# Performance work log

Hardware: AMD Instinct MI355X
Metric: run time of the kernel (lower is better)

Reference implementation:

```python
import jax, jax.numpy as jnp
import numpy as np

B = 8192
D1 = 1024
D2 = 1024
H = 4096  # subnet hidden width
SCALE_LIMIT = 1.0


def _mlp(x, W1, b1, W2, b2):
    # Linear -> ReLU -> Linear
    return jnp.maximum(x @ W1 + b1, 0.0) @ W2 + b2


def setup_inputs() -> dict:
    key = jax.random.key(0)
    ks = jax.random.split(key, 17)
    inp = {"x": jax.random.normal(ks[0], (B, D1 + D2), dtype=jnp.float32)}
    # four subnets: s1,t1 map d2->d1 ; s2,t2 map d1->d2
    specs = {"s1": (D2, D1), "t1": (D2, D1), "s2": (D1, D2), "t2": (D1, D2)}
    i = 1
    for name, (din, dout) in specs.items():
        inp[f"{name}_W1"] = 0.02 * jax.random.normal(ks[i], (din, H), dtype=jnp.float32); i += 1
        inp[f"{name}_b1"] = jnp.zeros((H,), dtype=jnp.float32)
        inp[f"{name}_W2"] = 0.02 * jax.random.normal(ks[i], (H, dout), dtype=jnp.float32); i += 1
        inp[f"{name}_b2"] = jnp.zeros((dout,), dtype=jnp.float32)
    return inp


def reference(x,
              s1_W1, s1_b1, s1_W2, s1_b2,
              t1_W1, t1_b1, t1_W2, t1_b2,
              s2_W1, s2_b1, s2_W2, s2_b2,
              t2_W1, t2_b1, t2_W2, t2_b2):
    x1, x2 = x[:, :D1], x[:, D1:]
    # first half-step: update x1 conditioned on x2
    s2v = jnp.tanh(_mlp(x2, s1_W1, s1_b1, s1_W2, s1_b2)) * SCALE_LIMIT  # [B, D1]
    t2v = _mlp(x2, t1_W1, t1_b1, t1_W2, t1_b2)                          # [B, D1]
    y1 = x1 * jnp.exp(s2v) + t2v
    # second half-step: update x2 conditioned on y1
    s1v = jnp.tanh(_mlp(y1, s2_W1, s2_b1, s2_W2, s2_b2)) * SCALE_LIMIT  # [B, D2]
    t1v = _mlp(y1, t2_W1, t2_b1, t2_W2, t2_b2)                          # [B, D2]
    y2 = x2 * jnp.exp(s1v) + t1v
    y = jnp.concatenate([y1, y2], axis=1)  # [B, D1+D2]
    # exact triangular-coupling log-det (what the autograd loop computes per-sample)
    log_det = jnp.sum(s2v, axis=1) + jnp.sum(s1v, axis=1)  # [B]
    return y, log_det
```

## Files before the change

### kernel.cpp

```cpp
#include <hip/hip_runtime.h>
#include <cstdint>
#include <cstddef>

#define BDIM 8192
#define D1 1024
#define HDIM 4096

typedef __attribute__((ext_vector_type(8))) short short8;
typedef __attribute__((ext_vector_type(4))) float f32x4;
typedef __attribute__((ext_vector_type(4))) unsigned short u16x4;

__device__ inline void async_load16(const void* g, void* l) {
  __builtin_amdgcn_global_load_lds(
      (const __attribute__((address_space(1))) void*)g,
      (__attribute__((address_space(3))) void*)l,
      16 , 0 , 0 );
}

__device__ inline unsigned short f2bf(float f) {
  union { float f; uint32_t u; } v; v.f = f;
  uint32_t u = v.u;
  uint32_t r = u + 0x7FFFu + ((u >> 16) & 1u);
  return (unsigned short)(r >> 16);
}
__device__ inline float bf2f(unsigned short u) {
  union { uint32_t u; float f; } v; v.u = (uint32_t)u << 16; return v.f;
}

__global__ __launch_bounds__(512, 2)
void gemm8(const unsigned short* __restrict__ A0,
           const unsigned short* __restrict__ A1, int lda,
           const unsigned short* __restrict__ B0,
           const unsigned short* __restrict__ B1,
           const float* __restrict__ bias0, const float* __restrict__ bias1,
           unsigned short* __restrict__ C0, unsigned short* __restrict__ C1,
           int ldc, int K, int relu) {
  __shared__ __align__(16) unsigned short smem[65536];

  const int z = blockIdx.z;
  const unsigned short* A  = z ? A1 : A0;
  const unsigned short* Bw = z ? B1 : B0;
  const float* biasP       = z ? bias1 : bias0;
  unsigned short* C        = z ? C1 : C0;

  const int nX  = gridDim.x;
  const int nwg = gridDim.x * gridDim.y;
  const int bid = blockIdx.y * gridDim.x + blockIdx.x;
  const int q = nwg >> 3, r = nwg & 7;
  const int xcd = bid & 7, rest = bid >> 3;
  const int wg = (xcd < r ? xcd * (q + 1) : r * (q + 1) + (xcd - r) * q) + rest;
  const int tm = wg / nX, tn = wg % nX;
  const int m0 = tm * 256, n0 = tn * 256;

  const int tid  = threadIdx.x;
  const int wave = tid >> 6, lane = tid & 63;
  const int quad = lane >> 4, l15 = lane & 15;
  const int wm = wave >> 2, wn = wave & 3;

  const int sr    = tid >> 2;
  const int sslot = (tid & 3) ^ ((tid >> 3) & 3);
  const unsigned short* gA = A  + (long)(m0 + sr) * lda + sslot * 8;
  const unsigned short* gB = Bw + (long)(n0 + sr) * K   + sslot * 8;

  const int rdoff = l15 * 32 + ((quad ^ ((l15 >> 1) & 3)) << 3);

  f32x4 acc[8][4] = {};
  const int NT = K >> 5;

#define STAGE_A(SB, KT) { \
  unsigned short* lw = smem + (SB)*8192 + wave*512; \
  const unsigned short* g = gA + (long)(KT)*32; \
  async_load16(g, lw); \
  async_load16(g + 128*(long)lda, lw + 4096); }

#define STAGE_B(SB, KT) { \
  unsigned short* lw = smem + 32768 + (SB)*8192 + wave*512; \
  const unsigned short* g = gB + (long)(KT)*32; \
  async_load16(g, lw); \
  async_load16(g + 128*(long)K, lw + 4096); }

#define READ_AL(d, BUF) { \
  const unsigned short* p = smem + (BUF)*8192 + wm*4096 + rdoff; \
  d[0] = *(const short8*)(p);        d[1] = *(const short8*)(p + 512); \
  d[2] = *(const short8*)(p + 1024); d[3] = *(const short8*)(p + 1536); }

#define READ_AH(d, BUF) { \
  const unsigned short* p = smem + (BUF)*8192 + wm*4096 + 2048 + rdoff; \
  d[0] = *(const short8*)(p);        d[1] = *(const short8*)(p + 512); \
  d[2] = *(const short8*)(p + 1024); d[3] = *(const short8*)(p + 1536); }

#define READ_B(d, BUF) { \
  const unsigned short* p = smem + 32768 + (BUF)*8192 + wn*2048 + rdoff; \
  d[0] = *(const short8*)(p);        d[1] = *(const short8*)(p + 512); \
  d[2] = *(const short8*)(p + 1024); d[3] = *(const short8*)(p + 1536); }

#define MFMA16L(AV, BV) \
  _Pragma("unroll") \
  for (int mt = 0; mt < 4; ++mt) { \
    _Pragma("unroll") \
    for (int nt = 0; nt < 4; ++nt) { \
      acc[mt][nt] = __builtin_amdgcn_mfma_f32_16x16x32_bf16( \
          AV[mt], BV[nt], acc[mt][nt], 0, 0, 0); \
    } }

#define MFMA16H(AV, BV) \
  _Pragma("unroll") \
  for (int mt = 0; mt < 4; ++mt) { \
    _Pragma("unroll") \
    for (int nt = 0; nt < 4; ++nt) { \
      acc[4 + mt][nt] = __builtin_amdgcn_mfma_f32_16x16x32_bf16( \
          AV[mt], BV[nt], acc[4 + mt][nt], 0, 0, 0); \
    } }

#define BARRIER() asm volatile("s_barrier" ::: "memory")
#define VMCNT8()  asm volatile("s_waitcnt vmcnt(8)" ::: "memory")

#define STEP(BUF, SB, KTS, CA, CB, NA, NBv) { \
  short8 h4[4]; \
  READ_AH(h4, BUF); \
  { const int kt = (KTS) < NT ? (KTS) : NT - 1; \
    STAGE_A(SB, kt); STAGE_B(SB, kt); } \
  __builtin_amdgcn_s_setprio(1); MFMA16L(CA, CB); __builtin_amdgcn_s_setprio(0); \
  VMCNT8(); \
  BARRIER(); \
  READ_AL(NA, ((BUF) + 1) & 3); READ_B(NBv, ((BUF) + 1) & 3); \
  __builtin_amdgcn_s_setprio(1); MFMA16H(h4, CB); __builtin_amdgcn_s_setprio(0); \
}

  short8 pa[4], pb[4], qa[4], qb[4];

  STAGE_A(0, 0); STAGE_B(0, 0);
  STAGE_A(1, 1); STAGE_B(1, 1);
  STAGE_A(2, 2); STAGE_B(2, 2);
  VMCNT8();
  BARRIER();
  READ_AL(pa, 0); READ_B(pb, 0);

#pragma unroll 1
  for (int t = 0; t < NT; t += 4) {
    STEP(0, 3, t + 3, pa, pb, qa, qb);
    STEP(1, 0, t + 4, qa, qb, pa, pb);
    STEP(2, 1, t + 5, pa, pb, qa, qb);
    STEP(3, 2, t + 6, qa, qb, pa, pb);
  }

  asm volatile("s_waitcnt vmcnt(0)" ::: "memory");
  BARRIER();

  unsigned short* sc = smem + wave * 8192;
#pragma unroll
  for (int nt = 0; nt < 4; ++nt) {
    const int col = n0 + wn * 64 + nt * 16 + l15;
    const float bv = biasP[col];
#pragma unroll
    for (int mt = 0; mt < 8; ++mt) {
#pragma unroll
      for (int rr = 0; rr < 4; ++rr) {
        const int lrow = mt * 16 + quad * 4 + rr;
        float v = acc[mt][nt][rr] + bv;
        if (relu) v = v > 0.f ? v : 0.f;
        sc[lrow * 64 + ((nt * 16 + l15) ^ (((lrow >> 2) & 3) << 4))] = f2bf(v);
      }
    }
  }
  const long rowbase = m0 + wm * 128;
  const int colbase  = n0 + wn * 64;
#pragma unroll
  for (int i = 0; i < 16; ++i) {
    const int L   = i * 1024 + lane * 16;
    const int row = L >> 7;
    const int sp  = (L & 127) >> 4;
    const int cg  = sp ^ ((((row) >> 2) & 3) << 1);
    short8 v = *(const short8*)&sc[row * 64 + sp * 8];
    *(short8*)&C[(rowbase + row) * (long)ldc + colbase + cg * 8] = v;
  }

#undef STAGE_A
#undef STAGE_B
#undef READ_AL
#undef READ_AH
#undef READ_B
#undef MFMA16L
#undef MFMA16H
#undef BARRIER
#undef VMCNT8
#undef STEP
}

__global__ __launch_bounds__(256)
void couple(const unsigned short* sb, const unsigned short* __restrict__ tb,
            const float* __restrict__ x, float* __restrict__ y,
            unsigned short* y1b, float* __restrict__ ld,
            long growoff, int xoff, int addld) {
  __shared__ float wsum[4];
  const int row = blockIdx.x;
  const long grow = growoff + row;
  const int c = threadIdx.x * 4;

  u16x4 sv4 = *(const u16x4*)&sb[(long)row * 1024 + c];
  u16x4 tv4 = *(const u16x4*)&tb[(long)row * 1024 + c];
  f32x4 xv  = *(const f32x4*)&x[grow * 2048 + xoff + c];
  f32x4 yv;
  unsigned short yb[4];
  float rs = 0.f;
#pragma unroll
  for (int j = 0; j < 4; ++j) {
    float s  = bf2f(sv4[j]);
    float t  = bf2f(tv4[j]);
    float sv = tanhf(s);
    rs += sv;
    float yy = xv[j] * __expf(sv) + t;
    yv[j] = yy;
    yb[j] = f2bf(yy);
  }
  *(f32x4*)&y[grow * 2048 + xoff + c] = yv;
  if (y1b) {
    u16x4 o; o[0] = yb[0]; o[1] = yb[1]; o[2] = yb[2]; o[3] = yb[3];
    *(u16x4*)&y1b[(long)row * 1024 + c] = o;
  }
#pragma unroll
  for (int o = 32; o > 0; o >>= 1) rs += __shfl_down(rs, o);
  const int wv = threadIdx.x >> 6, ln = threadIdx.x & 63;
  if (ln == 0) wsum[wv] = rs;
  __syncthreads();
  if (threadIdx.x == 0) {
    float tot = wsum[0] + wsum[1] + wsum[2] + wsum[3];
    if (addld) ld[grow] += tot; else ld[grow] = tot;
  }
}

__global__ __launch_bounds__(256)
void transpose_cast4(const float* __restrict__ s0, const float* __restrict__ s1,
                     const float* __restrict__ s2, const float* __restrict__ s3,
                     unsigned short* __restrict__ d0, unsigned short* __restrict__ d1,
                     unsigned short* __restrict__ d2, unsigned short* __restrict__ d3,
                     int R, int C) {
  __shared__ float tile[32][33];
  const int bz = blockIdx.z;
  const float* in = bz == 0 ? s0 : bz == 1 ? s1 : bz == 2 ? s2 : s3;
  unsigned short* out = bz == 0 ? d0 : bz == 1 ? d1 : bz == 2 ? d2 : d3;
  const int bx = blockIdx.x * 32;
  const int by = blockIdx.y * 32;
  const int tx = threadIdx.x & 31;
  const int ty = threadIdx.x >> 5;
  for (int j = ty; j < 32; j += 8)
    tile[j][tx] = in[(long)(by + j) * C + bx + tx];
  __syncthreads();
  for (int j = ty; j < 32; j += 8)
    out[(long)(bx + j) * R + by + tx] = f2bf(tile[tx][j]);
}

__global__ __launch_bounds__(256)
void cast_x2(const float* __restrict__ x, unsigned short* __restrict__ x2b) {
  long i = (long)blockIdx.x * 256 + threadIdx.x;
  long row = i >> 10, col = i & 1023;
  x2b[i] = f2bf(x[row * (2 * D1) + D1 + col]);
}

extern "C" void kernel_launch(void* const* d_in, const int* in_sizes, int n_in,
                              void* d_out, int out_size, void* d_ws, size_t ws_size,
                              hipStream_t stream) {
  const float* x     = (const float*)d_in[0];
  const float* s1_W1 = (const float*)d_in[1];
  const float* s1_b1 = (const float*)d_in[2];
  const float* s1_W2 = (const float*)d_in[3];
  const float* s1_b2 = (const float*)d_in[4];
  const float* t1_W1 = (const float*)d_in[5];
  const float* t1_b1 = (const float*)d_in[6];
  const float* t1_W2 = (const float*)d_in[7];
  const float* t1_b2 = (const float*)d_in[8];
  const float* s2_W1 = (const float*)d_in[9];
  const float* s2_b1 = (const float*)d_in[10];
  const float* s2_W2 = (const float*)d_in[11];
  const float* s2_b2 = (const float*)d_in[12];
  const float* t2_W1 = (const float*)d_in[13];
  const float* t2_b1 = (const float*)d_in[14];
  const float* t2_W2 = (const float*)d_in[15];
  const float* t2_b2 = (const float*)d_in[16];

  const size_t MB = 1024UL * 1024UL;
  float* y_out  = (float*)d_out;
  float* ld_out = (float*)d_out + (long)BDIM * (2 * D1);
  char* ws = (char*)d_ws;

  if (ws_size >= 192 * MB) {
    unsigned short* w1a = (unsigned short*)(ws + 0 * MB);
    unsigned short* w1b = (unsigned short*)(ws + 8 * MB);
    unsigned short* w2a = (unsigned short*)(ws + 16 * MB);
    unsigned short* w2b = (unsigned short*)(ws + 24 * MB);
    unsigned short* x2b = (unsigned short*)(ws + 32 * MB);
    unsigned short* tb  = (unsigned short*)(ws + 48 * MB);
    unsigned short* h   = (unsigned short*)(ws + 64 * MB);

    cast_x2<<<(BDIM * D1) / 256, 256, 0, stream>>>(x, x2b);
    transpose_cast4<<<dim3(HDIM / 32, D1 / 32, 2), 256, 0, stream>>>(
        s1_W1, t1_W1, s1_W1, s1_W1, w1a, w1b, w1a, w1a, D1, HDIM);
    transpose_cast4<<<dim3(D1 / 32, HDIM / 32, 2), 256, 0, stream>>>(
        s1_W2, t1_W2, s1_W2, s1_W2, w2a, w2b, w2a, w2a, HDIM, D1);

    gemm8<<<dim3(16, 32, 2), 512, 0, stream>>>(x2b, x2b, D1, w1a, w1b,
        s1_b1, t1_b1, h, h + 4096, 2 * HDIM, D1, 1);
    transpose_cast4<<<dim3(HDIM / 32, D1 / 32, 2), 256, 0, stream>>>(
        s2_W1, t2_W1, s2_W1, s2_W1, w1a, w1b, w1a, w1a, D1, HDIM);
    gemm8<<<dim3(4, 32, 2), 512, 0, stream>>>(h, h + 4096, 2 * HDIM, w2a, w2b,
        s1_b2, t1_b2, x2b , tb, D1, HDIM, 0);
    transpose_cast4<<<dim3(D1 / 32, HDIM / 32, 2), 256, 0, stream>>>(
        s2_W2, t2_W2, s2_W2, s2_W2, w2a, w2b, w2a, w2a, HDIM, D1);
    couple<<<BDIM, 256, 0, stream>>>(x2b, tb, x, y_out, x2b ,
                                     ld_out, 0, 0, 0);
    gemm8<<<dim3(16, 32, 2), 512, 0, stream>>>(x2b, x2b, D1, w1a, w1b,
        s2_b1, t2_b1, h, h + 4096, 2 * HDIM, D1, 1);
    gemm8<<<dim3(4, 32, 2), 512, 0, stream>>>(h, h + 4096, 2 * HDIM, w2a, w2b,
        s2_b2, t2_b2, x2b , tb, D1, HDIM, 0);
    couple<<<BDIM, 256, 0, stream>>>(x2b, tb, x, y_out, nullptr, ld_out, 0, D1, 1);
  } else {
    int NC = 2;
    while (NC < 16) {
      size_t need = 80 * MB + (16 * MB) / NC + (128 * MB) / NC;
      if (need <= ws_size) break;
      NC <<= 1;
    }
    const int Mrows = BDIM / NC;
    unsigned short* w1s1 = (unsigned short*)(ws + 0 * MB);
    unsigned short* w1t1 = (unsigned short*)(ws + 8 * MB);
    unsigned short* w1s2 = (unsigned short*)(ws + 16 * MB);
    unsigned short* w1t2 = (unsigned short*)(ws + 24 * MB);
    unsigned short* w2s1 = (unsigned short*)(ws + 32 * MB);
    unsigned short* w2t1 = (unsigned short*)(ws + 40 * MB);
    unsigned short* w2s2 = (unsigned short*)(ws + 48 * MB);
    unsigned short* w2t2 = (unsigned short*)(ws + 56 * MB);
    unsigned short* x2b  = (unsigned short*)(ws + 64 * MB);
    unsigned short* tb   = (unsigned short*)(ws + 80 * MB);
    unsigned short* h    = (unsigned short*)(ws + 80 * MB + (16 * MB) / NC);

    cast_x2<<<(BDIM * D1) / 256, 256, 0, stream>>>(x, x2b);
    transpose_cast4<<<dim3(HDIM / 32, D1 / 32, 4), 256, 0, stream>>>(
        s1_W1, t1_W1, s2_W1, t2_W1, w1s1, w1t1, w1s2, w1t2, D1, HDIM);
    transpose_cast4<<<dim3(D1 / 32, HDIM / 32, 4), 256, 0, stream>>>(
        s1_W2, t1_W2, s2_W2, t2_W2, w2s1, w2t1, w2s2, w2t2, HDIM, D1);

    for (int c = 0; c < NC; ++c) {
      const long moff = (long)c * Mrows;
      unsigned short* xA = x2b + moff * D1;
      gemm8<<<dim3(16, Mrows / 256, 2), 512, 0, stream>>>(xA, xA, D1, w1s1, w1t1,
          s1_b1, t1_b1, h, h + 4096, 2 * HDIM, D1, 1);
      gemm8<<<dim3(4, Mrows / 256, 2), 512, 0, stream>>>(h, h + 4096, 2 * HDIM,
          w2s1, w2t1, s1_b2, t1_b2, xA, tb, D1, HDIM, 0);
      couple<<<Mrows, 256, 0, stream>>>(xA, tb, x, y_out, xA, ld_out, moff, 0, 0);
      gemm8<<<dim3(16, Mrows / 256, 2), 512, 0, stream>>>(xA, xA, D1, w1s2, w1t2,
          s2_b1, t2_b1, h, h + 4096, 2 * HDIM, D1, 1);
      gemm8<<<dim3(4, Mrows / 256, 2), 512, 0, stream>>>(h, h + 4096, 2 * HDIM,
          w2s2, w2t2, s2_b2, t2_b2, xA, tb, D1, HDIM, 0);
      couple<<<Mrows, 256, 0, stream>>>(xA, tb, x, y_out, nullptr, ld_out, moff, D1, 1);
    }
  }
}
```

Measured before the change: 784.1 us.

## Use 4-wave GEMM blocks with 128x128 per-wave tiles and simpler pipeline

The bf16 GEMM moves from 8 waves per 256x256 tile to 4 waves, each computing a 128x128 sub-tile with 64 accumulators, so each LDS fragment read feeds more MFMAs. The staging loads four rows per thread per stage, the split low/high half-step interleave is replaced by a single read-then-compute step, and the epilogue swizzle is widened. The aim is less LDS read traffic per MFMA, traded for far more registers (256 accumulator floats plus 32 fragment registers), one block per CU, and less latency hiding.

Result: slower. 1.245 ms (+58.7%).

```diff
diff --git a/kernel.cpp b/kernel.cpp
--- a/kernel.cpp
+++ b/kernel.cpp
@@ -27,7 +27,7 @@
   union { uint32_t u; float f; } v; v.u = (uint32_t)u << 16; return v.f;
 }
 
-__global__ __launch_bounds__(512, 2)
+__global__ __launch_bounds__(256, 1)
 void gemm8(const unsigned short* __restrict__ A0,
            const unsigned short* __restrict__ A1, int lda,
            const unsigned short* __restrict__ B0,
@@ -55,102 +55,83 @@
   const int tid  = threadIdx.x;
   const int wave = tid >> 6, lane = tid & 63;
   const int quad = lane >> 4, l15 = lane & 15;
-  const int wm = wave >> 2, wn = wave & 3;
+  const int wm = wave >> 1, wn = wave & 1;
 
   const int sr    = tid >> 2;
   const int sslot = (tid & 3) ^ ((tid >> 3) & 3);
   const unsigned short* gA = A  + (long)(m0 + sr) * lda + sslot * 8;
   const unsigned short* gB = Bw + (long)(n0 + sr) * K   + sslot * 8;
 
-  const int rdoff = l15 * 32 + ((quad ^ ((l15 >> 1) & 3)) << 3);
-
-  f32x4 acc[8][4] = {};
+  const int swz = ((quad ^ ((l15 >> 1) & 3)) << 3);
+  const unsigned short* aRd = smem + wm * 4096 + l15 * 32 + swz;
+  const unsigned short* bRd = smem + 32768 + wn * 4096 + l15 * 32 + swz;
+
+  f32x4 acc[8][8] = {};
   const int NT = K >> 5;
 
-#define STAGE_A(SB, KT) { \
-  unsigned short* lw = smem + (SB)*8192 + wave*512; \
-  const unsigned short* g = gA + (long)(KT)*32; \
-  async_load16(g, lw); \
-  async_load16(g + 128*(long)lda, lw + 4096); }
-
-#define STAGE_B(SB, KT) { \
-  unsigned short* lw = smem + 32768 + (SB)*8192 + wave*512; \
-  const unsigned short* g = gB + (long)(KT)*32; \
-  async_load16(g, lw); \
-  async_load16(g + 128*(long)K, lw + 4096); }
-
-#define READ_AL(d, BUF) { \
-  const unsigned short* p = smem + (BUF)*8192 + wm*4096 + rdoff; \
-  d[0] = *(const short8*)(p);        d[1] = *(const short8*)(p + 512); \
-  d[2] = *(const short8*)(p + 1024); d[3] = *(const short8*)(p + 1536); }
-
-#define READ_AH(d, BUF) { \
-  const unsigned short* p = smem + (BUF)*8192 + wm*4096 + 2048 + rdoff; \
-  d[0] = *(const short8*)(p);        d[1] = *(const short8*)(p + 512); \
-  d[2] = *(const short8*)(p + 1024); d[3] = *(const short8*)(p + 1536); }
-
-#define READ_B(d, BUF) { \
-  const unsigned short* p = smem + 32768 + (BUF)*8192 + wn*2048 + rdoff; \
-  d[0] = *(const short8*)(p);        d[1] = *(const short8*)(p + 512); \
-  d[2] = *(const short8*)(p + 1024); d[3] = *(const short8*)(p + 1536); }
-
-#define MFMA16L(AV, BV) \
+#define STAGE(SB, KT) { \
+  const int kt_ = (KT) < NT ? (KT) : NT - 1; \
+  const unsigned short* ga_ = gA + (long)kt_ * 32; \
+  const unsigned short* gb_ = gB + (long)kt_ * 32; \
+  unsigned short* la_ = smem + (SB)*8192 + wave*512; \
+  unsigned short* lb_ = smem + 32768 + (SB)*8192 + wave*512; \
+  async_load16(ga_,                    la_); \
+  async_load16(ga_ +  64*(long)lda,    la_ + 2048); \
+  async_load16(ga_ + 128*(long)lda,    la_ + 4096); \
+  async_load16(ga_ + 192*(long)lda,    la_ + 6144); \
+  async_load16(gb_,                    lb_); \
+  async_load16(gb_ +  64*(long)K,      lb_ + 2048); \
+  async_load16(gb_ + 128*(long)K,      lb_ + 4096); \
+  async_load16(gb_ + 192*(long)K,      lb_ + 6144); }
+
+#define READ8(d, BASE, BUF) { \
   _Pragma("unroll") \
-  for (int mt = 0; mt < 4; ++mt) { \
+  for (int fr = 0; fr < 8; ++fr) \
+    d[fr] = *(const short8*)((BASE) + (BUF)*8192 + fr*512); }
+
+#define MFMA64(CA, CB) \
+  _Pragma("unroll") \
+  for (int mt = 0; mt < 8; ++mt) { \
     _Pragma("unroll") \
-    for (int nt = 0; nt < 4; ++nt) { \
+    for (int nt = 0; nt < 8; ++nt) { \
       acc[mt][nt] = __builtin_amdgcn_mfma_f32_16x16x32_bf16( \
-          AV[mt], BV[nt], acc[mt][nt], 0, 0, 0); \
+          CA[mt], CB[nt], acc[mt][nt], 0, 0, 0); \
     } }
 
-#define MFMA16H(AV, BV) \
-  _Pragma("unroll") \
-  for (int mt = 0; mt < 4; ++mt) { \
-    _Pragma("unroll") \
-    for (int nt = 0; nt < 4; ++nt) { \
-      acc[4 + mt][nt] = __builtin_amdgcn_mfma_f32_16x16x32_bf16( \
-          AV[mt], BV[nt], acc[4 + mt][nt], 0, 0, 0); \
-    } }
-
 #define BARRIER() asm volatile("s_barrier" ::: "memory")
-#define VMCNT8()  asm volatile("s_waitcnt vmcnt(8)" ::: "memory")
-
-#define STEP(BUF, SB, KTS, CA, CB, NA, NBv) { \
-  short8 h4[4]; \
-  READ_AH(h4, BUF); \
-  { const int kt = (KTS) < NT ? (KTS) : NT - 1; \
-    STAGE_A(SB, kt); STAGE_B(SB, kt); } \
-  __builtin_amdgcn_s_setprio(1); MFMA16L(CA, CB); __builtin_amdgcn_s_setprio(0); \
-  VMCNT8(); \
+#define VMCNT16() asm volatile("s_waitcnt vmcnt(16)" ::: "memory")
+
+#define STEP(BUF, NXB, SB, CA, CB, NA, NB, KTX) { \
+  STAGE(SB, KTX); \
+  VMCNT16(); \
   BARRIER(); \
-  READ_AL(NA, ((BUF) + 1) & 3); READ_B(NBv, ((BUF) + 1) & 3); \
-  __builtin_amdgcn_s_setprio(1); MFMA16H(h4, CB); __builtin_amdgcn_s_setprio(0); \
-}
-
-  short8 pa[4], pb[4], qa[4], qb[4];
-
-  STAGE_A(0, 0); STAGE_B(0, 0);
-  STAGE_A(1, 1); STAGE_B(1, 1);
-  STAGE_A(2, 2); STAGE_B(2, 2);
-  VMCNT8();
+  READ8(NA, aRd, NXB); READ8(NB, bRd, NXB); \
+  __builtin_amdgcn_sched_barrier(0); \
+  MFMA64(CA, CB); \
+}
+
+  short8 pa[8], pb[8], qa[8], qb[8];
+
+  STAGE(0, 0); STAGE(1, 1); STAGE(2, 2);
+  VMCNT16();
   BARRIER();
-  READ_AL(pa, 0); READ_B(pb, 0);
+  READ8(pa, aRd, 0); READ8(pb, bRd, 0);
 
 #pragma unroll 1
   for (int t = 0; t < NT; t += 4) {
-    STEP(0, 3, t + 3, pa, pb, qa, qb);
-    STEP(1, 0, t + 4, qa, qb, pa, pb);
-    STEP(2, 1, t + 5, pa, pb, qa, qb);
-    STEP(3, 2, t + 6, qa, qb, pa, pb);
+    STEP(0, 1, 3, pa, pb, qa, qb, t + 3);
+    STEP(1, 2, 0, qa, qb, pa, pb, t + 4);
+    STEP(2, 3, 1, pa, pb, qa, qb, t + 5);
+    STEP(3, 0, 2, qa, qb, pa, pb, t + 6);
   }
 
   asm volatile("s_waitcnt vmcnt(0)" ::: "memory");
   BARRIER();
 
-  unsigned short* sc = smem + wave * 8192;
-#pragma unroll
-  for (int nt = 0; nt < 4; ++nt) {
-    const int col = n0 + wn * 64 + nt * 16 + l15;
+  unsigned short* sc = smem + wave * 16384;
+#pragma unroll
+  for (int nt = 0; nt < 8; ++nt) {
+    const int col = n0 + wn * 128 + nt * 16 + l15;
     const float bv = biasP[col];
 #pragma unroll
     for (int mt = 0; mt < 8; ++mt) {
@@ -159,31 +140,27 @@
         const int lrow = mt * 16 + quad * 4 + rr;
         float v = acc[mt][nt][rr] + bv;
         if (relu) v = v > 0.f ? v : 0.f;
-        sc[lrow * 64 + ((nt * 16 + l15) ^ (((lrow >> 2) & 3) << 4))] = f2bf(v);
+        sc[lrow * 128 + ((nt * 16 + l15) ^ (((lrow >> 2) & 7) << 4))] = f2bf(v);
       }
     }
   }
   const long rowbase = m0 + wm * 128;
-  const int colbase  = n0 + wn * 64;
-#pragma unroll
-  for (int i = 0; i < 16; ++i) {
+  const int colbase  = n0 + wn * 128;
+#pragma unroll
+  for (int i = 0; i < 32; ++i) {
     const int L   = i * 1024 + lane * 16;
-    const int row = L >> 7;
-    const int sp  = (L & 127) >> 4;
-    const int cg  = sp ^ ((((row) >> 2) & 3) << 1);
-    short8 v = *(const short8*)&sc[row * 64 + sp * 8];
+    const int row = L >> 8;
+    const int sp  = (L & 255) >> 4;
+    const int cg  = sp ^ (((row >> 2) & 7) << 1);
+    short8 v = *(const short8*)&sc[row * 128 + sp * 8];
     *(short8*)&C[(rowbase + row) * (long)ldc + colbase + cg * 8] = v;
   }
 
-#undef STAGE_A
-#undef STAGE_B
-#undef READ_AL
-#undef READ_AH
-#undef READ_B
-#undef MFMA16L
-#undef MFMA16H
+#undef STAGE
+#undef READ8
+#undef MFMA64
 #undef BARRIER
-#undef VMCNT8
+#undef VMCNT16
 #undef STEP
 }
 
@@ -298,19 +275,19 @@
     transpose_cast4<<<dim3(D1 / 32, HDIM / 32, 2), 256, 0, stream>>>(
         s1_W2, t1_W2, s1_W2, s1_W2, w2a, w2b, w2a, w2a, HDIM, D1);
 
-    gemm8<<<dim3(16, 32, 2), 512, 0, stream>>>(x2b, x2b, D1, w1a, w1b,
+    gemm8<<<dim3(16, 32, 2), 256, 0, stream>>>(x2b, x2b, D1, w1a, w1b,
         s1_b1, t1_b1, h, h + 4096, 2 * HDIM, D1, 1);
     transpose_cast4<<<dim3(HDIM / 32, D1 / 32, 2), 256, 0, stream>>>(
         s2_W1, t2_W1, s2_W1, s2_W1, w1a, w1b, w1a, w1a, D1, HDIM);
-    gemm8<<<dim3(4, 32, 2), 512, 0, stream>>>(h, h + 4096, 2 * HDIM, w2a, w2b,
+    gemm8<<<dim3(4, 32, 2), 256, 0, stream>>>(h, h + 4096, 2 * HDIM, w2a, w2b,
         s1_b2, t1_b2, x2b , tb, D1, HDIM, 0);
     transpose_cast4<<<dim3(D1 / 32, HDIM / 32, 2), 256, 0, stream>>>(
         s2_W2, t2_W2, s2_W2, s2_W2, w2a, w2b, w2a, w2a, HDIM, D1);
     couple<<<BDIM, 256, 0, stream>>>(x2b, tb, x, y_out, x2b ,
                                      ld_out, 0, 0, 0);
-    gemm8<<<dim3(16, 32, 2), 512, 0, stream>>>(x2b, x2b, D1, w1a, w1b,
+    gemm8<<<dim3(16, 32, 2), 256, 0, stream>>>(x2b, x2b, D1, w1a, w1b,
         s2_b1, t2_b1, h, h + 4096, 2 * HDIM, D1, 1);
-    gemm8<<<dim3(4, 32, 2), 512, 0, stream>>>(h, h + 4096, 2 * HDIM, w2a, w2b,
+    gemm8<<<dim3(4, 32, 2), 256, 0, stream>>>(h, h + 4096, 2 * HDIM, w2a, w2b,
         s2_b2, t2_b2, x2b , tb, D1, HDIM, 0);
     couple<<<BDIM, 256, 0, stream>>>(x2b, tb, x, y_out, nullptr, ld_out, 0, D1, 1);
   } else {
@@ -342,14 +319,14 @@
     for (int c = 0; c < NC; ++c) {
       const long moff = (long)c * Mrows;
       unsigned short* xA = x2b + moff * D1;
-      gemm8<<<dim3(16, Mrows / 256, 2), 512, 0, stream>>>(xA, xA, D1, w1s1, w1t1,
+      gemm8<<<dim3(16, Mrows / 256, 2), 256, 0, stream>>>(xA, xA, D1, w1s1, w1t1,
           s1_b1, t1_b1, h, h + 4096, 2 * HDIM, D1, 1);
-      gemm8<<<dim3(4, Mrows / 256, 2), 512, 0, stream>>>(h, h + 4096, 2 * HDIM,
+      gemm8<<<dim3(4, Mrows / 256, 2), 256, 0, stream>>>(h, h + 4096, 2 * HDIM,
           w2s1, w2t1, s1_b2, t1_b2, xA, tb, D1, HDIM, 0);
       couple<<<Mrows, 256, 0, stream>>>(xA, tb, x, y_out, xA, ld_out, moff, 0, 0);
-      gemm8<<<dim3(16, Mrows / 256, 2), 512, 0, stream>>>(xA, xA, D1, w1s2, w1t2,
+      gemm8<<<dim3(16, Mrows / 256, 2), 256, 0, stream>>>(xA, xA, D1, w1s2, w1t2,
           s2_b1, t2_b1, h, h + 4096, 2 * HDIM, D1, 1);
-      gemm8<<<dim3(4, Mrows / 256, 2), 512, 0, stream>>>(h, h + 4096, 2 * HDIM,
+      gemm8<<<dim3(4, Mrows / 256, 2), 256, 0, stream>>>(h, h + 4096, 2 * HDIM,
           w2s2, w2t2, s2_b2, t2_b2, xA, tb, D1, HDIM, 0);
       couple<<<Mrows, 256, 0, stream>>>(xA, tb, x, y_out, nullptr, ld_out, moff, D1, 1);
     }
```
